# Optimization experiments

Hardware: AMD Instinct MI355X
Metric: run time of the kernel (lower is better)

## Reference

```python
import jax, jax.numpy as jnp
import numpy as np


def setup_inputs() -> dict:
    key = jax.random.key(0)
    k1, k2 = jax.random.split(key)
    B, G, P = 32, 64, 256
    pred_patches = jax.random.normal(k1, (B, G, P, 3), dtype=jnp.float32)
    target_patches = jax.random.normal(k2, (B, G, P, 3), dtype=jnp.float32)
    return {"pred_patches": pred_patches, "target_patches": target_patches}


def reference(pred_patches, target_patches):
    b, g, p, _ = pred_patches.shape
    pred = pred_patches.reshape(b * g, p, 3)    # (BG, P, 3)
    tgt = target_patches.reshape(b * g, p, 3)   # (BG, P, 3)
    # Squared euclidean distance via ||p||^2 + ||q||^2 - 2 p.q (matches cdist(p=2)**2)
    pn = jnp.sum(pred * pred, axis=-1)          # (BG, P)
    tn = jnp.sum(tgt * tgt, axis=-1)            # (BG, P)
    cross = jnp.einsum('bpd,bqd->bpq', pred, tgt)  # (BG, P, P)
    dist2 = jnp.maximum(pn[:, :, None] + tn[:, None, :] - 2.0 * cross, 0.0)
    forward_dist = jnp.min(dist2, axis=2).mean(axis=1)   # nearest target for each pred point
    backward_dist = jnp.min(dist2, axis=1).mean(axis=1)  # nearest pred for each target point
    per_patch = forward_dist + backward_dist             # (BG,)
    return jnp.mean(per_patch)  # reduction='mean' over batch*patches
```

## Files before the change

### kernel.cpp

```cpp
#include <hip/hip_runtime.h>


#define NPATCH 2048
#define NPTS   256

__global__ __launch_bounds__(128) void chamfer_patch_kernel(
    const float* __restrict__ pred,
    const float* __restrict__ tgt,
    float* __restrict__ partial)
{
    __shared__ float4 pPk[NPTS];
    __shared__ float4 tPk[NPTS];
    __shared__ float red[2];

    const int patch = blockIdx.x;
    const int tid   = threadIdx.x;
    const float* __restrict__ pb = pred + (size_t)patch * (NPTS * 3);
    const float* __restrict__ tb = tgt  + (size_t)patch * (NPTS * 3);

    #pragma unroll
    for (int q = 0; q < 2; ++q) {
        const int p = tid * 2 + q;
        float x = pb[3 * p + 0];
        float y = pb[3 * p + 1];
        float z = pb[3 * p + 2];
        pPk[p] = make_float4(-2.0f * x, -2.0f * y, -2.0f * z,
                             x * x + y * y + z * z);
        x = tb[3 * p + 0];
        y = tb[3 * p + 1];
        z = tb[3 * p + 2];
        tPk[p] = make_float4(-2.0f * x, -2.0f * y, -2.0f * z,
                             x * x + y * y + z * z);
    }
    __syncthreads();

    const int wave = tid >> 6;
    const int lane = tid & 63;

    float qx[4], qy[4], qz[4], qn[4], m[4];
    float s = 0.0f;

    if (wave == 0) {
        #pragma unroll
        for (int q = 0; q < 4; ++q) {
            const float4 v = pPk[lane + 64 * q];
            qx[q] = -0.5f * v.x;
            qy[q] = -0.5f * v.y;
            qz[q] = -0.5f * v.z;
            qn[q] = v.w;
            m[q]  = 1e30f;
        }
        #pragma unroll 4
        for (int j = 0; j < NPTS; ++j) {
            const float4 t = tPk[j];
            #pragma unroll
            for (int q = 0; q < 4; ++q) {
                float d = fmaf(qx[q], t.x, t.w);
                d = fmaf(qy[q], t.y, d);
                d = fmaf(qz[q], t.z, d);
                m[q] = fminf(m[q], d);
            }
        }
        #pragma unroll
        for (int q = 0; q < 4; ++q) s += fmaxf(qn[q] + m[q], 0.0f);
    } else {
        #pragma unroll
        for (int q = 0; q < 4; ++q) {
            const float4 v = tPk[lane + 64 * q];
            qx[q] = -0.5f * v.x;
            qy[q] = -0.5f * v.y;
            qz[q] = -0.5f * v.z;
            qn[q] = v.w;
            m[q]  = 1e30f;
        }
        #pragma unroll 4
        for (int j = 0; j < NPTS; ++j) {
            const float4 t = pPk[j];
            #pragma unroll
            for (int q = 0; q < 4; ++q) {
                float d = fmaf(qx[q], t.x, t.w);
                d = fmaf(qy[q], t.y, d);
                d = fmaf(qz[q], t.z, d);
                m[q] = fminf(m[q], d);
            }
        }
        #pragma unroll
        for (int q = 0; q < 4; ++q) s += fmaxf(qn[q] + m[q], 0.0f);
    }

    #pragma unroll
    for (int off = 32; off > 0; off >>= 1)
        s += __shfl_down(s, off, 64);
    if (lane == 0) red[wave] = s;
    __syncthreads();
    if (tid == 0) partial[patch] = red[0] + red[1];
}

__global__ __launch_bounds__(256) void chamfer_reduce_kernel(
    const float* __restrict__ partial,
    float* __restrict__ out)
{
    __shared__ float red[4];
    const int tid = threadIdx.x;
    float s = 0.0f;
    #pragma unroll
    for (int i = tid; i < NPATCH; i += 256) s += partial[i];
    #pragma unroll
    for (int off = 32; off > 0; off >>= 1)
        s += __shfl_down(s, off, 64);
    if ((tid & 63) == 0) red[tid >> 6] = s;
    __syncthreads();
    if (tid == 0)
        out[0] = (red[0] + red[1] + red[2] + red[3]) *
                 (1.0f / ((float)NPTS * (float)NPATCH));
}

extern "C" void kernel_launch(void* const* d_in, const int* in_sizes, int n_in,
                              void* d_out, int out_size, void* d_ws, size_t ws_size,
                              hipStream_t stream) {
    const float* pred = (const float*)d_in[0];
    const float* tgt  = (const float*)d_in[1];
    float* partial    = (float*)d_ws;
    float* out        = (float*)d_out;

    chamfer_patch_kernel<<<NPATCH, 128, 0, stream>>>(pred, tgt, partial);
    chamfer_reduce_kernel<<<1, 256, 0, stream>>>(partial, out);
}
```

Before: 83.96 us.

## Split chamfer directions across blocks and stream source points from global memory

```diff
diff --git a/kernel.cpp b/kernel.cpp
--- a/kernel.cpp
+++ b/kernel.cpp
@@ -4,96 +4,71 @@
 #define NPATCH 2048
 #define NPTS   256
 
-__global__ __launch_bounds__(128) void chamfer_patch_kernel(
+__global__ __launch_bounds__(128, 8) void chamfer_dir_kernel(
     const float* __restrict__ pred,
     const float* __restrict__ tgt,
     float* __restrict__ partial)
 {
-    __shared__ float4 pPk[NPTS];
-    __shared__ float4 tPk[NPTS];
-    __shared__ float red[2];
+    __shared__ float mbuf[2][NPTS];
 
     const int patch = blockIdx.x;
-    const int tid   = threadIdx.x;
-    const float* __restrict__ pb = pred + (size_t)patch * (NPTS * 3);
-    const float* __restrict__ tb = tgt  + (size_t)patch * (NPTS * 3);
+    const int dir   = blockIdx.y;
+    const float* __restrict__ qb = (dir == 0 ? pred : tgt) + (size_t)patch * (NPTS * 3);
+    const float* __restrict__ sb = (dir == 0 ? tgt : pred) + (size_t)patch * (NPTS * 3);
 
-    #pragma unroll
-    for (int q = 0; q < 2; ++q) {
-        const int p = tid * 2 + q;
-        float x = pb[3 * p + 0];
-        float y = pb[3 * p + 1];
-        float z = pb[3 * p + 2];
-        pPk[p] = make_float4(-2.0f * x, -2.0f * y, -2.0f * z,
-                             x * x + y * y + z * z);
-        x = tb[3 * p + 0];
-        y = tb[3 * p + 1];
-        z = tb[3 * p + 2];
-        tPk[p] = make_float4(-2.0f * x, -2.0f * y, -2.0f * z,
-                             x * x + y * y + z * z);
-    }
-    __syncthreads();
-
-    const int wave = tid >> 6;
+    const int tid  = threadIdx.x;
+    const int wave = __builtin_amdgcn_readfirstlane(tid >> 6);
     const int lane = tid & 63;
 
     float qx[4], qy[4], qz[4], qn[4], m[4];
-    float s = 0.0f;
+#pragma unroll
+    for (int q = 0; q < 4; ++q) {
+        const int p = lane + 64 * q;
+        const float x = qb[3 * p + 0];
+        const float y = qb[3 * p + 1];
+        const float z = qb[3 * p + 2];
+        qx[q] = -2.0f * x;
+        qy[q] = -2.0f * y;
+        qz[q] = -2.0f * z;
+        qn[q] = fmaf(z, z, fmaf(y, y, x * x));
+        m[q]  = 1e30f;
+    }
+
+    const float* __restrict__ s0 = sb + wave * (NPTS / 2) * 3;
+#pragma unroll 4
+    for (int jp = 0; jp < NPTS / 4; ++jp) {
+        const float ax = s0[6 * jp + 0];
+        const float ay = s0[6 * jp + 1];
+        const float az = s0[6 * jp + 2];
+        const float bx = s0[6 * jp + 3];
+        const float by = s0[6 * jp + 4];
+        const float bz = s0[6 * jp + 5];
+        const float an = fmaf(az, az, fmaf(ay, ay, ax * ax));
+        const float bn = fmaf(bz, bz, fmaf(by, by, bx * bx));
+#pragma unroll
+        for (int q = 0; q < 4; ++q) {
+            const float da = fmaf(qx[q], ax, fmaf(qy[q], ay, fmaf(qz[q], az, an)));
+            const float db = fmaf(qx[q], bx, fmaf(qy[q], by, fmaf(qz[q], bz, bn)));
+            m[q] = fminf(m[q], fminf(da, db));
+        }
+    }
+
+#pragma unroll
+    for (int q = 0; q < 4; ++q) mbuf[wave][lane + 64 * q] = m[q];
+    __syncthreads();
 
     if (wave == 0) {
-        #pragma unroll
+        float s = 0.0f;
+#pragma unroll
         for (int q = 0; q < 4; ++q) {
-            const float4 v = pPk[lane + 64 * q];
-            qx[q] = -0.5f * v.x;
-            qy[q] = -0.5f * v.y;
-            qz[q] = -0.5f * v.z;
-            qn[q] = v.w;
-            m[q]  = 1e30f;
+            const float mm = fminf(mbuf[0][lane + 64 * q], mbuf[1][lane + 64 * q]);
+            s += fmaxf(qn[q] + mm, 0.0f);
         }
-        #pragma unroll 4
-        for (int j = 0; j < NPTS; ++j) {
-            const float4 t = tPk[j];
-            #pragma unroll
-            for (int q = 0; q < 4; ++q) {
-                float d = fmaf(qx[q], t.x, t.w);
-                d = fmaf(qy[q], t.y, d);
-                d = fmaf(qz[q], t.z, d);
-                m[q] = fminf(m[q], d);
-            }
-        }
-        #pragma unroll
-        for (int q = 0; q < 4; ++q) s += fmaxf(qn[q] + m[q], 0.0f);
-    } else {
-        #pragma unroll
-        for (int q = 0; q < 4; ++q) {
-            const float4 v = tPk[lane + 64 * q];
-            qx[q] = -0.5f * v.x;
-            qy[q] = -0.5f * v.y;
-            qz[q] = -0.5f * v.z;
-            qn[q] = v.w;
-            m[q]  = 1e30f;
-        }
-        #pragma unroll 4
-        for (int j = 0; j < NPTS; ++j) {
-            const float4 t = pPk[j];
-            #pragma unroll
-            for (int q = 0; q < 4; ++q) {
-                float d = fmaf(qx[q], t.x, t.w);
-                d = fmaf(qy[q], t.y, d);
-                d = fmaf(qz[q], t.z, d);
-                m[q] = fminf(m[q], d);
-            }
-        }
-        #pragma unroll
-        for (int q = 0; q < 4; ++q) s += fmaxf(qn[q] + m[q], 0.0f);
+#pragma unroll
+        for (int off = 32; off > 0; off >>= 1)
+            s += __shfl_down(s, off, 64);
+        if (lane == 0) partial[patch * 2 + dir] = s;
     }
-
-    #pragma unroll
-    for (int off = 32; off > 0; off >>= 1)
-        s += __shfl_down(s, off, 64);
-    if (lane == 0) red[wave] = s;
-    __syncthreads();
-    if (tid == 0) partial[patch] = red[0] + red[1];
 }
 
 __global__ __launch_bounds__(256) void chamfer_reduce_kernel(
@@ -103,9 +78,9 @@
     __shared__ float red[4];
     const int tid = threadIdx.x;
     float s = 0.0f;
-    #pragma unroll
-    for (int i = tid; i < NPATCH; i += 256) s += partial[i];
-    #pragma unroll
+#pragma unroll
+    for (int i = tid; i < NPATCH * 2; i += 256) s += partial[i];
+#pragma unroll
     for (int off = 32; off > 0; off >>= 1)
         s += __shfl_down(s, off, 64);
     if ((tid & 63) == 0) red[tid >> 6] = s;
@@ -123,6 +98,6 @@
     float* partial    = (float*)d_ws;
     float* out        = (float*)d_out;
 
-    chamfer_patch_kernel<<<NPATCH, 128, 0, stream>>>(pred, tgt, partial);
+    chamfer_dir_kernel<<<dim3(NPATCH, 2), 128, 0, stream>>>(pred, tgt, partial);
     chamfer_reduce_kernel<<<1, 256, 0, stream>>>(partial, out);
 }
```

New measurement: 95.25 us. 13.4% more time.
